# Kernel optimization log

Measured on AMD Instinct MI355X. Metric: run time of the kernel, lower is better.

Reference implementation:

```python
import jax, jax.numpy as jnp
import numpy as np

HID = 128          # args.hid
HEADS = 1          # args.head (forced: concat=True and classifier expects 3*hid)
C = HID            # out_channels per head
ND, NPR, NCL = 4096, 20000, 1024
E_DD, E_DP, E_CP = 500_000, 1_000_000, 500_000
B = 8192
SLOPE = 0.2        # GATConv negative_slope default


def _gat(x_src, x_dst, src, dst, W, a_src, a_dst, bias, num_dst,
         edge_attr=None, W_edge=None, a_edge=None):
    # PyG GATConv: shared lin for src/dst (in_channels is int)
    hs = (x_src @ W).reshape(-1, HEADS, C)            # [Ns,H,C]
    hd = (x_dst @ W).reshape(-1, HEADS, C)            # [Nd,H,C]
    e = jnp.sum(hs * a_src, -1)[src] + jnp.sum(hd * a_dst, -1)[dst]  # [E,H]
    if edge_attr is not None:
        ee = (edge_attr @ W_edge).reshape(-1, HEADS, C)
        e = e + jnp.sum(ee * a_edge, -1)
    e = jnp.where(e > 0, e, SLOPE * e)                # leaky_relu
    emax = jax.ops.segment_max(e, dst, num_segments=num_dst)
    ex = jnp.exp(e - emax[dst])
    denom = jax.ops.segment_sum(ex, dst, num_segments=num_dst)
    alpha = ex / (denom[dst] + 1e-16)                 # PyG softmax eps
    out = jax.ops.segment_sum(hs[src] * alpha[:, :, None], dst, num_segments=num_dst)
    return out.reshape(num_dst, HEADS * C) + bias


def _l2n(x):
    return x / jnp.maximum(jnp.linalg.norm(x, axis=1, keepdims=True), 1e-12)


def setup_inputs() -> dict:
    key = jax.random.key(0)
    ks = iter(jax.random.split(key, 48))

    def nrm(shape, s=0.1):
        return jax.random.normal(next(ks), shape, jnp.float32) * s

    inp = {
        'x_drug': jnp.arange(ND, dtype=jnp.int32),
        'x_protein': jnp.arange(NPR, dtype=jnp.int32),
        'x_cell': jnp.arange(NCL, dtype=jnp.int32),
        'ei_dd': jax.random.randint(next(ks), (2, E_DD), 0, ND),
        'edge_attr_dd': jax.random.normal(next(ks), (E_DD, 1), jnp.float32),
        'src_dp': jax.random.randint(next(ks), (E_DP,), 0, NPR),
        'dst_dp': jax.random.randint(next(ks), (E_DP,), 0, ND),
        'src_cp': jax.random.randint(next(ks), (E_CP,), 0, NPR),
        'dst_cp': jax.random.randint(next(ks), (E_CP,), 0, NCL),
        'drug1': jax.random.randint(next(ks), (B,), 0, ND),
        'drug2': jax.random.randint(next(ks), (B,), 0, ND),
        'cell': jax.random.randint(next(ks), (B,), 0, NCL),
        # embedding tables
        'drug_emb': nrm((ND, HID), 1.0),
        'protein_emb': nrm((NPR, HID), 1.0),
        'cell_emb': nrm((NCL, HID), 1.0),
        # GAT d-d (edge_dim=1)
        'W_dd': nrm((HID, HEADS * C)), 'a_src_dd': nrm((HEADS, C)), 'a_dst_dd': nrm((HEADS, C)),
        'bias_dd': jnp.zeros((HEADS * C,), jnp.float32),
        'W_edge_dd': nrm((1, HEADS * C)), 'a_edge_dd': nrm((HEADS, C)),
        # GAT protein->drug
        'W_dp': nrm((HID, HEADS * C)), 'a_src_dp': nrm((HEADS, C)), 'a_dst_dp': nrm((HEADS, C)),
        'bias_dp': jnp.zeros((HEADS * C,), jnp.float32),
        # GAT protein->cell
        'W_cp': nrm((HID, HEADS * C)), 'a_src_cp': nrm((HEADS, C)), 'a_dst_cp': nrm((HEADS, C)),
        'bias_cp': jnp.zeros((HEADS * C,), jnp.float32),
        # classifier: 3h -> 6h -> 2h -> 2
        'W1': nrm((3 * HID, 6 * HID)), 'b1': jnp.zeros((6 * HID,), jnp.float32),
        'W2': nrm((6 * HID, 2 * HID)), 'b2': jnp.zeros((2 * HID,), jnp.float32),
        'W3': nrm((2 * HID, 2)), 'b3': jnp.zeros((2,), jnp.float32),
    }
    return inp


def reference(x_drug, x_protein, x_cell, ei_dd, edge_attr_dd, src_dp, dst_dp,
              src_cp, dst_cp, drug1, drug2, cell, drug_emb, protein_emb, cell_emb,
              W_dd, a_src_dd, a_dst_dd, bias_dd, W_edge_dd, a_edge_dd,
              W_dp, a_src_dp, a_dst_dp, bias_dp,
              W_cp, a_src_cp, a_dst_cp, bias_cp,
              W1, b1, W2, b2, W3, b3):
    h_d = drug_emb[x_drug]
    h_p = protein_emb[x_protein]
    h_c = cell_emb[x_cell]

    # d-d: add self-loops with edge_attr fill_value='mean' (PyG default)
    src, dst = ei_dd[0], ei_dd[1]
    deg = jax.ops.segment_sum(jnp.ones((E_DD,), jnp.float32), dst, num_segments=ND)
    mean_attr = jax.ops.segment_sum(edge_attr_dd, dst, num_segments=ND) / jnp.maximum(deg, 1.0)[:, None]
    loops = jnp.arange(ND, dtype=src.dtype)
    src2 = jnp.concatenate([src, loops])
    dst2 = jnp.concatenate([dst, loops])
    attr2 = jnp.concatenate([edge_attr_dd, mean_attr], 0)

    out_dd = _gat(h_d, h_d, src2, dst2, W_dd, a_src_dd, a_dst_dd, bias_dd, ND,
                  attr2, W_edge_dd, a_edge_dd)
    out_dp = _gat(h_p, h_d, src_dp, dst_dp, W_dp, a_src_dp, a_dst_dp, bias_dp, ND)
    out_cp = _gat(h_p, h_c, src_cp, dst_cp, W_cp, a_src_cp, a_dst_cp, bias_cp, NCL)

    drug = jax.nn.relu(out_dd + out_dp)   # HeteroConv aggr='sum', then F.relu
    cellx = jax.nn.relu(out_cp)

    hid = jnp.concatenate([_l2n(drug[drug1]), _l2n(drug[drug2]), _l2n(cellx[cell])], 1)
    h = jax.nn.relu(hid @ W1 + b1)        # dropout = identity in eval
    h = jax.nn.relu(h @ W2 + b2)
    return h @ W3 + b3
```

## Files before the change

kernel.cpp:

```cpp
#include <hip/hip_runtime.h>
#include <hip/hip_bf16.h>

#define HIDC 128
typedef __hip_bfloat16 bf16;
typedef __attribute__((ext_vector_type(8))) short short8;
typedef __attribute__((ext_vector_type(4))) float floatx4;

#define CHUNK 4096

__device__ __forceinline__ short f2b(float f) {
    unsigned int u = __builtin_bit_cast(unsigned int, f);
    u += 0x7fff + ((u >> 16) & 1);
    return (short)(u >> 16);
}

__device__ __forceinline__ uint packe(int s, float ev) {
    float w = __expf(ev);
    return ((uint)s << 16) | (uint)(unsigned short)f2b(w);
}

__global__ void __launch_bounds__(256) r15_prep(
    int* __restrict__ zptr, int zwords, int nzb,
    const float* __restrict__ W_dd, const float* __restrict__ W_dp, const float* __restrict__ W_cp,
    const float* __restrict__ a0, const float* __restrict__ a1, const float* __restrict__ a2,
    const float* __restrict__ a3, const float* __restrict__ a4, const float* __restrict__ a5,
    const float* __restrict__ W_edge, const float* __restrict__ a_edge,
    float* __restrict__ wa, float* __restrict__ c_edge,
    const float* __restrict__ W1, short* __restrict__ Wt1, int nT1,
    const float* __restrict__ W2, short* __restrict__ Wt2)
{
    int b = blockIdx.x;
    int tid = threadIdx.x;
    if (b < nzb) {
        int i = b * 256 + tid;
        if (i < zwords) zptr[i] = 0;
        return;
    }
    b -= nzb;
    if (b < 7) {
        __shared__ float as[HIDC];
        int k = tid;
        if (b < 6) {
            const float* W = (b < 2) ? W_dd : (b < 4) ? W_dp : W_cp;
            const float* a = (b == 0) ? a0 : (b == 1) ? a1 : (b == 2) ? a2 : (b == 3) ? a3 : (b == 4) ? a4 : a5;
            if (k < HIDC) as[k] = a[k];
            __syncthreads();
            if (k < HIDC) {
                float s = 0.f;
#pragma unroll 8
                for (int c = 0; c < HIDC; c++) s = fmaf(W[k * HIDC + c], as[c], s);
                wa[b * HIDC + k] = s;
            }
        } else {
            if (k < HIDC) as[k] = W_edge[k] * a_edge[k];
            __syncthreads();
#pragma unroll
            for (int off = 64; off > 0; off >>= 1) { if (k < off) as[k] += as[k + off]; __syncthreads(); }
            if (k == 0) c_edge[0] = as[0];
        }
        return;
    }
    b -= 7;
    const float* W; short* Wt; int K, N, k0, n0;
    if (b < nT1) { W = W1; Wt = Wt1; K = 384; N = 768; k0 = (b / 24) * 32; n0 = (b % 24) * 32; }
    else { b -= nT1; W = W2; Wt = Wt2; K = 768; N = 256; k0 = (b / 8) * 32; n0 = (b % 8) * 32; }
    __shared__ short T[32 * 34];
    int cc = tid & 31, rr = tid >> 5;
#pragma unroll
    for (int it = 0; it < 4; it++) {
        int r = it * 8 + rr;
        T[r * 34 + cc] = f2b(W[(size_t)(k0 + r) * N + n0 + cc]);
    }
    __syncthreads();
#pragma unroll
    for (int it = 0; it < 4; it++) {
        int r = it * 8 + rr;
        Wt[(size_t)(n0 + r) * K + k0 + cc] = T[cc * 34 + r];
    }
}

__global__ void __launch_bounds__(256) r15_scalars(
    const float* __restrict__ drug_emb, const float* __restrict__ prot_emb, const float* __restrict__ cell_emb,
    const int* __restrict__ x_drug, const int* __restrict__ x_prot, const int* __restrict__ x_cell,
    const float* __restrict__ wa,
    float* __restrict__ ssrc_dd, float* __restrict__ sdst_dd, float* __restrict__ sdst_dp,
    float* __restrict__ ssrc_dp, float* __restrict__ ssrc_cp, float* __restrict__ sdst_cp,
    int nd, int npr, int ncl)
{
    int g = blockIdx.x * 4 + (threadIdx.x >> 6);
    int l = threadIdx.x & 63;
    const float2* wa2 = (const float2*)wa;
    if (g < nd) {
        int id = x_drug[g];
        float2 e = ((const float2*)drug_emb)[(size_t)id * 64 + l];
        float2 w0 = wa2[0 * 64 + l], w1 = wa2[1 * 64 + l], w3 = wa2[3 * 64 + l];
        float p0 = e.x * w0.x + e.y * w0.y;
        float p1 = e.x * w1.x + e.y * w1.y;
        float p2 = e.x * w3.x + e.y * w3.y;
#pragma unroll
        for (int off = 32; off > 0; off >>= 1) {
            p0 += __shfl_xor(p0, off, 64);
            p1 += __shfl_xor(p1, off, 64);
            p2 += __shfl_xor(p2, off, 64);
        }
        if (l == 0) { ssrc_dd[g] = p0; sdst_dd[g] = p1; sdst_dp[g] = p2; }
    } else if (g < nd + npr) {
        int r = g - nd;
        int id = x_prot[r];
        float2 e = ((const float2*)prot_emb)[(size_t)id * 64 + l];
        float2 w2 = wa2[2 * 64 + l], w4 = wa2[4 * 64 + l];
        float p0 = e.x * w2.x + e.y * w2.y;
        float p1 = e.x * w4.x + e.y * w4.y;
#pragma unroll
        for (int off = 32; off > 0; off >>= 1) {
            p0 += __shfl_xor(p0, off, 64);
            p1 += __shfl_xor(p1, off, 64);
        }
        if (l == 0) { ssrc_dp[r] = p0; ssrc_cp[r] = p1; }
    } else if (g < nd + npr + ncl) {
        int r = g - nd - npr;
        int id = x_cell[r];
        float2 e = ((const float2*)cell_emb)[(size_t)id * 64 + l];
        float2 w5 = wa2[5 * 64 + l];
        float p0 = e.x * w5.x + e.y * w5.y;
#pragma unroll
        for (int off = 32; off > 0; off >>= 1) p0 += __shfl_xor(p0, off, 64);
        if (l == 0) sdst_cp[r] = p0;
    }
}

__global__ void __launch_bounds__(128) r15_node_gemm(
    const float* __restrict__ drug_emb, const int* __restrict__ x_drug,
    const float* __restrict__ W_dd, bf16* __restrict__ H_dd, int ndb,
    const float* __restrict__ prot_emb, const int* __restrict__ x_prot,
    const float* __restrict__ W_dp, const float* __restrict__ W_cp,
    bf16* __restrict__ H_dp, bf16* __restrict__ H_cp)
{
    __shared__ int ids[16];
    __shared__ float xs[16 * HIDC];
    int bb = blockIdx.x;
    bool isdrug = bb < ndb;
    int r0 = (isdrug ? bb : bb - ndb) * 16;
    const float* emb = isdrug ? drug_emb : prot_emb;
    const int* idx = isdrug ? x_drug : x_prot;
    int tid = threadIdx.x;
    if (tid < 16) ids[tid] = idx[r0 + tid];
    __syncthreads();
    for (int t = tid; t < 16 * HIDC; t += 128) {
        int r = t >> 7, k = t & 127;
        xs[t] = emb[(size_t)ids[r] * HIDC + k];
    }
    __syncthreads();
    int c = tid;
    if (isdrug) {
        float acc[16];
#pragma unroll
        for (int r = 0; r < 16; r++) acc[r] = 0.f;
        for (int k = 0; k < HIDC; k += 4) {
            float w0 = W_dd[(k + 0) * HIDC + c];
            float w1 = W_dd[(k + 1) * HIDC + c];
            float w2 = W_dd[(k + 2) * HIDC + c];
            float w3 = W_dd[(k + 3) * HIDC + c];
#pragma unroll
            for (int r = 0; r < 16; r++) {
                float4 x = *(const float4*)&xs[r * HIDC + k];
                acc[r] = fmaf(x.x, w0, fmaf(x.y, w1, fmaf(x.z, w2, fmaf(x.w, w3, acc[r]))));
            }
        }
#pragma unroll
        for (int r = 0; r < 16; r++) H_dd[(size_t)(r0 + r) * HIDC + c] = __float2bfloat16(acc[r]);
    } else {
        float accA[16], accB[16];
#pragma unroll
        for (int r = 0; r < 16; r++) { accA[r] = 0.f; accB[r] = 0.f; }
        for (int k = 0; k < HIDC; k += 2) {
            float a0 = W_dp[(k + 0) * HIDC + c];
            float a1 = W_dp[(k + 1) * HIDC + c];
            float b0 = W_cp[(k + 0) * HIDC + c];
            float b1 = W_cp[(k + 1) * HIDC + c];
#pragma unroll
            for (int r = 0; r < 16; r++) {
                float2 x = *(const float2*)&xs[r * HIDC + k];
                accA[r] = fmaf(x.x, a0, fmaf(x.y, a1, accA[r]));
                accB[r] = fmaf(x.x, b0, fmaf(x.y, b1, accB[r]));
            }
        }
#pragma unroll
        for (int r = 0; r < 16; r++) {
            H_dp[(size_t)(r0 + r) * HIDC + c] = __float2bfloat16(accA[r]);
            H_cp[(size_t)(r0 + r) * HIDC + c] = __float2bfloat16(accB[r]);
        }
    }
}

__global__ void __launch_bounds__(256) r15_edge_pass1(
    const int* __restrict__ dst_dd, const float* __restrict__ attr_dd, int E_dd, int nb_dd,
    const int* __restrict__ dst_dp, int E_dp, int nb_dp,
    const int* __restrict__ dst_cp, int E_cp,
    int nd, int ncl,
    int* __restrict__ cnt_dd, float* __restrict__ attr_sum,
    int* __restrict__ cnt_dp, int* __restrict__ cnt_cp,
    int* __restrict__ rank_dd, int* __restrict__ rank_dp, int* __restrict__ rank_cp)
{
    __shared__ int lcnt[4096];
    __shared__ float lattr[4096];
    int bid = blockIdx.x;
    const int* dst; const float* attr = nullptr; int E, e0, bins;
    int* gcnt; int* rank;
    if (bid < nb_dd) {
        dst = dst_dd; attr = attr_dd; E = E_dd; e0 = bid * CHUNK; bins = nd;
        gcnt = cnt_dd; rank = rank_dd;
    } else if (bid < nb_dd + nb_dp) {
        dst = dst_dp; E = E_dp; e0 = (bid - nb_dd) * CHUNK; bins = nd;
        gcnt = cnt_dp; rank = rank_dp;
    } else {
        dst = dst_cp; E = E_cp; e0 = (bid - nb_dd - nb_dp) * CHUNK; bins = ncl;
        gcnt = cnt_cp; rank = rank_cp;
    }
    int tid = threadIdx.x;
    for (int b = tid; b < bins; b += 256) { lcnt[b] = 0; if (attr) lattr[b] = 0.f; }
    __syncthreads();
    int e1 = min(e0 + CHUNK, E);
    for (int i = e0 + tid; i < e1; i += 256) {
        int d = dst[i];
        rank[i] = atomicAdd(&lcnt[d], 1);
        if (attr) atomicAdd(&lattr[d], attr[i]);
    }
    __syncthreads();
    for (int b = tid; b < bins; b += 256) {
        int c = lcnt[b];
        if (c > 0) {
            lcnt[b] = atomicAdd(&gcnt[b], c);
            if (attr) atomicAdd(&attr_sum[b], lattr[b]);
        }
    }
    __syncthreads();
    for (int i = e0 + tid; i < e1; i += 256) {
        rank[i] += lcnt[dst[i]];
    }
}

__global__ void __launch_bounds__(1024) r15_exscan3(
    const int* __restrict__ in0, int* __restrict__ out0, int n0,
    const int* __restrict__ in1, int* __restrict__ out1, int n1,
    const int* __restrict__ in2, int* __restrict__ out2, int n2)
{
    const int* in; int* out; int n; int inc;
    if (blockIdx.x == 0)      { in = in0; out = out0; n = n0; inc = 1; }
    else if (blockIdx.x == 1) { in = in1; out = out1; n = n1; inc = 0; }
    else                      { in = in2; out = out2; n = n2; inc = 0; }
    __shared__ int buf[1024];
    __shared__ int carry;
    int tid = threadIdx.x;
    if (tid == 0) carry = 0;
    __syncthreads();
    for (int base = 0; base < n; base += 1024) {
        int i = base + tid;
        int v = (i < n) ? (in[i] + inc) : 0;
        buf[tid] = v; __syncthreads();
        for (int off = 1; off < 1024; off <<= 1) {
            int t = (tid >= off) ? buf[tid - off] : 0;
            __syncthreads();
            buf[tid] += t;
            __syncthreads();
        }
        int c0 = carry;
        int incl = buf[tid];
        if (i < n) out[i] = c0 + incl - v;
        __syncthreads();
        if (tid == 1023) carry = c0 + buf[1023];
        __syncthreads();
    }
    if (tid == 0) out[n] = carry;
}

__global__ void r15_scatter(
    const int* __restrict__ ei_dd, const float* __restrict__ attr_dd, int E_dd, int nd,
    const int* __restrict__ src_dp, const int* __restrict__ dst_dp, int E_dp,
    const int* __restrict__ src_cp, const int* __restrict__ dst_cp, int E_cp,
    const int* __restrict__ rank_dd, const int* __restrict__ rank_dp, const int* __restrict__ rank_cp,
    const int* __restrict__ deg_dd, const float* __restrict__ attr_sum,
    const float* __restrict__ c_edge_ptr,
    const float* __restrict__ ssrc_dd, const float* __restrict__ sdst_dd,
    const float* __restrict__ ssrc_dp, const float* __restrict__ sdst_dp,
    const float* __restrict__ ssrc_cp, const float* __restrict__ sdst_cp,
    const int* __restrict__ rs_dd, const int* __restrict__ rs_dp, const int* __restrict__ rs_cp,
    uint* __restrict__ csr_dd, uint* __restrict__ csr_dp, uint* __restrict__ csr_cp)
{
    int i = blockIdx.x * 256 + threadIdx.x;
    if (i < E_dd) {
        int s = ei_dd[i], d = ei_dd[E_dd + i];
        float ev = ssrc_dd[s] + sdst_dd[d] + attr_dd[i] * c_edge_ptr[0];
        ev = (ev > 0.f) ? ev : 0.2f * ev;
        csr_dd[rs_dd[d] + rank_dd[i]] = packe(s, ev);
        return;
    }
    i -= E_dd;
    if (i < nd) {
        int d = i;
        int dg = deg_dd[d];
        float mean = attr_sum[d] / fmaxf((float)dg, 1.0f);
        float ev = ssrc_dd[d] + sdst_dd[d] + mean * c_edge_ptr[0];
        ev = (ev > 0.f) ? ev : 0.2f * ev;
        csr_dd[rs_dd[d] + dg] = packe(d, ev);
        return;
    }
    i -= nd;
    if (i < E_dp) {
        int d = dst_dp[i], s = src_dp[i];
        float ev = ssrc_dp[s] + sdst_dp[d];
        ev = (ev > 0.f) ? ev : 0.2f * ev;
        csr_dp[rs_dp[d] + rank_dp[i]] = packe(s, ev);
        return;
    }
    i -= E_dp;
    if (i < E_cp) {
        int d = dst_cp[i], s = src_cp[i];
        float ev = ssrc_cp[s] + sdst_cp[d];
        ev = (ev > 0.f) ? ev : 0.2f * ev;
        csr_cp[rs_cp[d] + rank_cp[i]] = packe(s, ev);
    }
}

__global__ void __launch_bounds__(256) r15_agg3(
    const int* __restrict__ rs_dd, const uint* __restrict__ csr_dd, const uint* __restrict__ Hdd,
    float* __restrict__ agg_dd, int nd,
    const int* __restrict__ rs_dp, const uint* __restrict__ csr_dp, const uint* __restrict__ Hdp,
    float* __restrict__ agg_dp,
    const int* __restrict__ rs_cp, const uint* __restrict__ csr_cp, const uint* __restrict__ Hcp,
    float* __restrict__ agg_cp, int R)
{
    int b = blockIdx.x;
    int slot = b & 7;
    int half = slot >> 2;
    int row_g = (b >> 3) * 4 + (slot & 3);
    if (row_g >= R) return;
    const int* rs; const uint* csr; const uint* H2; float* out; int row;
    if (row_g < nd)          { rs = rs_dd; csr = csr_dd; H2 = Hdd; out = agg_dd; row = row_g; }
    else if (row_g < 2 * nd) { rs = rs_dp; csr = csr_dp; H2 = Hdp; out = agg_dp; row = row_g - nd; }
    else                     { rs = rs_cp; csr = csr_cp; H2 = Hcp; out = agg_cp; row = row_g - 2 * nd; }
    int t = threadIdx.x;
    int c2 = t & 15, g = t >> 4;
    int s = rs[row], e = rs[row + 1];

    __shared__ float se[2][128];
    __shared__ int ss[2][128];
    const uint2* Hh = (const uint2*)H2 + half * 16 + c2;
    float acc[4] = {0.f, 0.f, 0.f, 0.f};
    float dsum = 0.f;
    int nchunks = (e - s + 127) >> 7;

    if (nchunks > 0 && t < min(128, e - s)) {
        uint pk = csr[s + t];
        float wv = __uint_as_float((pk & 0xffffu) << 16);
        se[0][t] = wv; ss[0][t] = (int)(pk >> 16);
        dsum += wv;
    }
    __syncthreads();
    for (int kk = 0; kk < nchunks; kk++) {
        int pb = kk & 1;
        if (kk + 1 < nchunks) {
            int nb2 = s + (kk + 1) * 128;
            int nlim = min(128, e - nb2);
            if (t < nlim) {
                uint pk = csr[nb2 + t];
                float wv = __uint_as_float((pk & 0xffffu) << 16);
                se[pb ^ 1][t] = wv; ss[pb ^ 1][t] = (int)(pk >> 16);
                dsum += wv;
            }
        }
        int lim = min(128, e - s - kk * 128);
        if (lim == 128) {
#pragma unroll 8
            for (int jj = 0; jj < 8; jj++) {
                int j = jj * 16 + g;
                uint2 u = Hh[(size_t)ss[pb][j] * 32];
                float w = se[pb][j];
                acc[0] = fmaf(w, __uint_as_float(u.x << 16), acc[0]);
                acc[1] = fmaf(w, __uint_as_float(u.x & 0xffff0000u), acc[1]);
                acc[2] = fmaf(w, __uint_as_float(u.y << 16), acc[2]);
                acc[3] = fmaf(w, __uint_as_float(u.y & 0xffff0000u), acc[3]);
            }
        } else {
            for (int j = g; j < lim; j += 16) {
                uint2 u = Hh[(size_t)ss[pb][j] * 32];
                float w = se[pb][j];
                acc[0] = fmaf(w, __uint_as_float(u.x << 16), acc[0]);
                acc[1] = fmaf(w, __uint_as_float(u.x & 0xffff0000u), acc[1]);
                acc[2] = fmaf(w, __uint_as_float(u.y << 16), acc[2]);
                acc[3] = fmaf(w, __uint_as_float(u.y & 0xffff0000u), acc[3]);
            }
        }
        __syncthreads();
    }

    float dwave = dsum;
#pragma unroll
    for (int off = 32; off > 0; off >>= 1) dwave += __shfl_xor(dwave, off, 64);
#pragma unroll
    for (int i = 0; i < 4; i++) {
        acc[i] += __shfl_xor(acc[i], 16, 64);
        acc[i] += __shfl_xor(acc[i], 32, 64);
    }
    __shared__ float rsum[4][64];
    __shared__ float dred[4];
    int w = t >> 6, l = t & 63;
    if (l == 0) dred[w] = dwave;
    if (l < 16) {
#pragma unroll
        for (int i = 0; i < 4; i++) rsum[w][l * 4 + i] = acc[i];
    }
    __syncthreads();
    if (t < 64) {
        float inv = 1.f / (dred[0] + dred[1] + dred[2] + dred[3] + 1e-16f);
        float v = rsum[0][t] + rsum[1][t] + rsum[2][t] + rsum[3][t];
        out[(size_t)row * HIDC + half * 64 + t] = v * inv;
    }
}

__global__ void __launch_bounds__(128) r15_fuse(
    const float* __restrict__ agg_dd, const float* __restrict__ bias_dd,
    const float* __restrict__ agg_dp, const float* __restrict__ bias_dp,
    float* __restrict__ drugN, int nd,
    const float* __restrict__ agg_cp, const float* __restrict__ bias_cp,
    float* __restrict__ cellN)
{
    int b = blockIdx.x, c = threadIdx.x;
    float v;
    float* outN;
    int d;
    if (b < nd) {
        d = b;
        v = agg_dd[(size_t)d * HIDC + c] + bias_dd[c] + agg_dp[(size_t)d * HIDC + c] + bias_dp[c];
        outN = drugN;
    } else {
        d = b - nd;
        v = agg_cp[(size_t)d * HIDC + c] + bias_cp[c];
        outN = cellN;
    }
    v = fmaxf(v, 0.f);
    __shared__ float red[HIDC];
    red[c] = v * v; __syncthreads();
#pragma unroll
    for (int off = 64; off > 0; off >>= 1) { if (c < off) red[c] += red[c + off]; __syncthreads(); }
    float nrm = fmaxf(sqrtf(red[0]), 1e-12f);
    outN[(size_t)d * HIDC + c] = v / nrm;
}

__global__ void __launch_bounds__(128) r15_gather_hid(
    const float* __restrict__ drugN, const float* __restrict__ cellN,
    const int* __restrict__ d1, const int* __restrict__ d2, const int* __restrict__ ce,
    short* __restrict__ hid)
{
    int b = blockIdx.x, c = threadIdx.x;
    hid[(size_t)b * 384 + c]       = f2b(drugN[(size_t)d1[b] * HIDC + c]);
    hid[(size_t)b * 384 + 128 + c] = f2b(drugN[(size_t)d2[b] * HIDC + c]);
    hid[(size_t)b * 384 + 256 + c] = f2b(cellN[(size_t)ce[b] * HIDC + c]);
}

template <int NB, int OUT_BF16>
__global__ void __launch_bounds__(256) r15_mgemm(
    const short* __restrict__ X, const short* __restrict__ Wt, const float* __restrict__ bias,
    void* __restrict__ Y, int M, int K, int N)
{
    constexpr int BN = NB * 16;
    __shared__ short As[128 * 40];
    __shared__ short Bs[BN * 40];
    int m0 = blockIdx.x * 128, n0 = blockIdx.y * BN;
    int tid = threadIdx.x;
    int w = tid >> 6, lane = tid & 63;
    int q = lane >> 4, t = lane & 15;
    int sr = tid >> 1, sc = tid & 1;

    floatx4 acc[2][NB];
#pragma unroll
    for (int i = 0; i < 2; i++)
#pragma unroll
        for (int c = 0; c < NB; c++) acc[i][c] = (floatx4){0.f, 0.f, 0.f, 0.f};

    for (int kt = 0; kt < K; kt += 32) {
        {
            const uint4* ga = (const uint4*)(X + (size_t)(m0 + sr) * K + kt + sc * 16);
            uint4 a0 = ga[0], a1 = ga[1];
            *(uint4*)&As[sr * 40 + sc * 16]     = a0;
            *(uint4*)&As[sr * 40 + sc * 16 + 8] = a1;
        }
        for (int tt = tid; tt < BN * 2; tt += 256) {
            int r = tt >> 1, h = tt & 1;
            const uint4* gb = (const uint4*)(Wt + (size_t)(n0 + r) * K + kt + h * 16);
            uint4 b0 = gb[0], b1 = gb[1];
            *(uint4*)&Bs[r * 40 + h * 16]     = b0;
            *(uint4*)&Bs[r * 40 + h * 16 + 8] = b1;
        }
        __syncthreads();
        short8 af[2], bf[NB];
#pragma unroll
        for (int i = 0; i < 2; i++)
            af[i] = *(const short8*)&As[(w * 32 + i * 16 + t) * 40 + q * 8];
#pragma unroll
        for (int c = 0; c < NB; c++)
            bf[c] = *(const short8*)&Bs[(c * 16 + t) * 40 + q * 8];
#pragma unroll
        for (int i = 0; i < 2; i++)
#pragma unroll
            for (int c = 0; c < NB; c++)
                acc[i][c] = __builtin_amdgcn_mfma_f32_16x16x32_bf16(af[i], bf[c], acc[i][c], 0, 0, 0);
        __syncthreads();
    }

    float bv[NB];
#pragma unroll
    for (int c = 0; c < NB; c++) bv[c] = bias[n0 + c * 16 + t];
#pragma unroll
    for (int i = 0; i < 2; i++) {
#pragma unroll
        for (int c = 0; c < NB; c++) {
#pragma unroll
            for (int ii = 0; ii < 4; ii++) {
                int m_g = m0 + w * 32 + i * 16 + q * 4 + ii;
                int n_g = n0 + c * 16 + t;
                float v = acc[i][c][ii] + bv[c];
                v = fmaxf(v, 0.f);
                if (OUT_BF16) ((short*)Y)[(size_t)m_g * N + n_g] = f2b(v);
                else          ((float*)Y)[(size_t)m_g * N + n_g] = v;
            }
        }
    }
}

__global__ void __launch_bounds__(256) r15_final(
    const float* __restrict__ h2, const float* __restrict__ W3, const float* __restrict__ b3,
    float* __restrict__ out)
{
    int row = blockIdx.x * 4 + (threadIdx.x >> 6);
    int lane = threadIdx.x & 63;
    float a0 = 0.f, a1 = 0.f;
    for (int k = lane; k < 256; k += 64) {
        float h = h2[(size_t)row * 256 + k];
        a0 = fmaf(h, W3[k * 2 + 0], a0);
        a1 = fmaf(h, W3[k * 2 + 1], a1);
    }
#pragma unroll
    for (int off = 32; off > 0; off >>= 1) {
        a0 += __shfl_down(a0, off, 64);
        a1 += __shfl_down(a1, off, 64);
    }
    if (lane == 0) {
        out[row * 2 + 0] = a0 + b3[0];
        out[row * 2 + 1] = a1 + b3[1];
    }
}

extern "C" void kernel_launch(void* const* d_in, const int* in_sizes, int n_in,
                              void* d_out, int out_size, void* d_ws, size_t ws_size,
                              hipStream_t stream)
{
    const int* x_drug      = (const int*)d_in[0];
    const int* x_protein   = (const int*)d_in[1];
    const int* x_cell      = (const int*)d_in[2];
    const int* ei_dd       = (const int*)d_in[3];
    const float* attr_dd   = (const float*)d_in[4];
    const int* src_dp      = (const int*)d_in[5];
    const int* dst_dp      = (const int*)d_in[6];
    const int* src_cp      = (const int*)d_in[7];
    const int* dst_cp      = (const int*)d_in[8];
    const int* drug1       = (const int*)d_in[9];
    const int* drug2       = (const int*)d_in[10];
    const int* cellb       = (const int*)d_in[11];
    const float* drug_emb  = (const float*)d_in[12];
    const float* protein_emb = (const float*)d_in[13];
    const float* cell_emb  = (const float*)d_in[14];
    const float* W_dd      = (const float*)d_in[15];
    const float* a_src_dd  = (const float*)d_in[16];
    const float* a_dst_dd  = (const float*)d_in[17];
    const float* bias_dd   = (const float*)d_in[18];
    const float* W_edge_dd = (const float*)d_in[19];
    const float* a_edge_dd = (const float*)d_in[20];
    const float* W_dp      = (const float*)d_in[21];
    const float* a_src_dp  = (const float*)d_in[22];
    const float* a_dst_dp  = (const float*)d_in[23];
    const float* bias_dp   = (const float*)d_in[24];
    const float* W_cp      = (const float*)d_in[25];
    const float* a_src_cp  = (const float*)d_in[26];
    const float* a_dst_cp  = (const float*)d_in[27];
    const float* bias_cp   = (const float*)d_in[28];
    const float* W1        = (const float*)d_in[29];
    const float* b1        = (const float*)d_in[30];
    const float* W2        = (const float*)d_in[31];
    const float* b2        = (const float*)d_in[32];
    const float* W3        = (const float*)d_in[33];
    const float* b3        = (const float*)d_in[34];

    const int ND  = in_sizes[0];
    const int NPR = in_sizes[1];
    const int NCL = in_sizes[2];
    const int E_DD = in_sizes[4];
    const int E_DP = in_sizes[5];
    const int E_CP = in_sizes[7];
    const int B    = in_sizes[9];
    const int E_DD2 = E_DD + ND;

    char* p = (char*)d_ws;
    auto carve = [&](size_t bytes) -> char* {
        char* r = p;
        p += (bytes + 255) & ~(size_t)255;
        return r;
    };
    char* zstart = p;
    int*   cnt_dd   = (int*)  carve((size_t)ND * 4);
    float* attr_sum = (float*)carve((size_t)ND * 4);
    int*   cnt_dp   = (int*)  carve((size_t)ND * 4);
    int*   cnt_cp   = (int*)  carve((size_t)NCL * 4);
    size_t zbytes = (size_t)(p - zstart);
    int*   rs_dd    = (int*)  carve((size_t)(ND + 1) * 4);
    int*   rs_dp    = (int*)  carve((size_t)(ND + 1) * 4);
    int*   rs_cp    = (int*)  carve((size_t)(NCL + 1) * 4);
    float* c_edge   = (float*)carve(256);
    float* wa       = (float*)carve(6 * HIDC * 4);
    bf16*  H_dd     = (bf16*) carve((size_t)ND * HIDC * 2);
    bf16*  H_dp     = (bf16*) carve((size_t)NPR * HIDC * 2);
    bf16*  H_cp     = (bf16*) carve((size_t)NPR * HIDC * 2);
    float* ssrc_dd  = (float*)carve((size_t)ND * 4);
    float* sdst_dd  = (float*)carve((size_t)ND * 4);
    float* ssrc_dp  = (float*)carve((size_t)NPR * 4);
    float* sdst_dp  = (float*)carve((size_t)ND * 4);
    float* ssrc_cp  = (float*)carve((size_t)NPR * 4);
    float* sdst_cp  = (float*)carve((size_t)NCL * 4);
    int*   rank_dd  = (int*)  carve((size_t)E_DD * 4);
    int*   rank_dp  = (int*)  carve((size_t)E_DP * 4);
    int*   rank_cp  = (int*)  carve((size_t)E_CP * 4);
    uint*  csr_dd   = (uint*) carve((size_t)E_DD2 * 4);
    uint*  csr_dp   = (uint*) carve((size_t)E_DP * 4);
    uint*  csr_cp   = (uint*) carve((size_t)E_CP * 4);
    float* agg_dd   = (float*)carve((size_t)ND * HIDC * 4);
    float* agg_dp   = (float*)carve((size_t)ND * HIDC * 4);
    float* agg_cp   = (float*)carve((size_t)NCL * HIDC * 4);
    float* drugN    = (float*)carve((size_t)ND * HIDC * 4);
    float* cellN    = (float*)carve((size_t)NCL * HIDC * 4);
    short* hidb     = (short*)carve((size_t)B * 384 * 2);
    short* h1b      = (short*)carve((size_t)B * 768 * 2);
    float* h2       = (float*)carve((size_t)B * 256 * 4);
    short* Wt1      = (short*)carve((size_t)384 * 768 * 2);
    short* Wt2      = (short*)carve((size_t)768 * 256 * 2);

    auto cdiv = [](int a, int b) { return (a + b - 1) / b; };

    int zwords = (int)(zbytes / 4);
    int nzb = cdiv(zwords, 256);
    int nT1 = (384 / 32) * (768 / 32);
    int nT2 = (768 / 32) * (256 / 32);
    r15_prep<<<nzb + 7 + nT1 + nT2, 256, 0, stream>>>(
        (int*)zstart, zwords, nzb,
        W_dd, W_dp, W_cp, a_src_dd, a_dst_dd, a_src_dp, a_dst_dp, a_src_cp, a_dst_cp,
        W_edge_dd, a_edge_dd, wa, c_edge, W1, Wt1, nT1, W2, Wt2);

    r15_node_gemm<<<ND / 16 + NPR / 16, 128, 0, stream>>>(
        drug_emb, x_drug, W_dd, H_dd, ND / 16,
        protein_emb, x_protein, W_dp, W_cp, H_dp, H_cp);
    r15_scalars<<<(ND + NPR + NCL) / 4, 256, 0, stream>>>(
        drug_emb, protein_emb, cell_emb, x_drug, x_protein, x_cell, wa,
        ssrc_dd, sdst_dd, sdst_dp, ssrc_dp, ssrc_cp, sdst_cp, ND, NPR, NCL);

    int nb_dd = cdiv(E_DD, CHUNK), nb_dp = cdiv(E_DP, CHUNK), nb_cp = cdiv(E_CP, CHUNK);
    r15_edge_pass1<<<nb_dd + nb_dp + nb_cp, 256, 0, stream>>>(
        ei_dd + E_DD, attr_dd, E_DD, nb_dd,
        dst_dp, E_DP, nb_dp,
        dst_cp, E_CP,
        ND, NCL,
        cnt_dd, attr_sum, cnt_dp, cnt_cp, rank_dd, rank_dp, rank_cp);
    r15_exscan3<<<3, 1024, 0, stream>>>(cnt_dd, rs_dd, ND, cnt_dp, rs_dp, ND, cnt_cp, rs_cp, NCL);
    r15_scatter<<<cdiv(E_DD + ND + E_DP + E_CP, 256), 256, 0, stream>>>(
        ei_dd, attr_dd, E_DD, ND, src_dp, dst_dp, E_DP, src_cp, dst_cp, E_CP,
        rank_dd, rank_dp, rank_cp, cnt_dd, attr_sum, c_edge,
        ssrc_dd, sdst_dd, ssrc_dp, sdst_dp, ssrc_cp, sdst_cp,
        rs_dd, rs_dp, rs_cp, csr_dd, csr_dp, csr_cp);

    {
        int R = 2 * ND + NCL;
        int G = cdiv(R, 4) * 8;
        r15_agg3<<<G, 256, 0, stream>>>(
            rs_dd, csr_dd, (const uint*)H_dd, agg_dd, ND,
            rs_dp, csr_dp, (const uint*)H_dp, agg_dp,
            rs_cp, csr_cp, (const uint*)H_cp, agg_cp, R);
    }

    r15_fuse<<<ND + NCL, 128, 0, stream>>>(agg_dd, bias_dd, agg_dp, bias_dp, drugN, ND,
                                           agg_cp, bias_cp, cellN);

    r15_gather_hid<<<B, 128, 0, stream>>>(drugN, cellN, drug1, drug2, cellb, hidb);
    {
        dim3 g1(B / 128, 768 / 128);
        r15_mgemm<8, 1><<<g1, 256, 0, stream>>>(hidb, Wt1, b1, (void*)h1b, B, 384, 768);
        dim3 g2(B / 128, 256 / 64);
        r15_mgemm<4, 0><<<g2, 256, 0, stream>>>(h1b, Wt2, b2, (void*)h2, B, 768, 256);
    }
    r15_final<<<B / 4, 256, 0, stream>>>(h2, W3, b3, (float*)d_out);
}
```

Before: 344.9 us.

## Merge edge histogram, node GEMM, weight transpose and scalars into one kernel

Combines four independent kernels (edge pass1 histogram/rank, node projection GEMM, MLP weight transpose, attention scalar dot products) into a single block-dispatched mega kernel. The node GEMM now uses 256-thread blocks covering 32 rows as two 16-row halves. This removes three kernel launches and their serialization gaps, letting independent work overlap across CUs. Trade-off: all blocks reserve 32KB shared memory, which may reduce occupancy for the lighter branches.

```diff
diff --git a/kernel.cpp b/kernel.cpp
--- a/kernel.cpp
+++ b/kernel.cpp
@@ -19,15 +19,13 @@
     return ((uint)s << 16) | (uint)(unsigned short)f2b(w);
 }
 
-__global__ void __launch_bounds__(256) r15_prep(
+__global__ void __launch_bounds__(256) r16_pre(
     int* __restrict__ zptr, int zwords, int nzb,
     const float* __restrict__ W_dd, const float* __restrict__ W_dp, const float* __restrict__ W_cp,
     const float* __restrict__ a0, const float* __restrict__ a1, const float* __restrict__ a2,
     const float* __restrict__ a3, const float* __restrict__ a4, const float* __restrict__ a5,
     const float* __restrict__ W_edge, const float* __restrict__ a_edge,
-    float* __restrict__ wa, float* __restrict__ c_edge,
-    const float* __restrict__ W1, short* __restrict__ Wt1, int nT1,
-    const float* __restrict__ W2, short* __restrict__ Wt2)
+    float* __restrict__ wa, float* __restrict__ c_edge)
 {
     int b = blockIdx.x;
     int tid = threadIdx.x;
@@ -37,210 +35,220 @@
         return;
     }
     b -= nzb;
-    if (b < 7) {
-        __shared__ float as[HIDC];
-        int k = tid;
-        if (b < 6) {
-            const float* W = (b < 2) ? W_dd : (b < 4) ? W_dp : W_cp;
-            const float* a = (b == 0) ? a0 : (b == 1) ? a1 : (b == 2) ? a2 : (b == 3) ? a3 : (b == 4) ? a4 : a5;
-            if (k < HIDC) as[k] = a[k];
-            __syncthreads();
-            if (k < HIDC) {
-                float s = 0.f;
+    __shared__ float as[HIDC];
+    int k = tid;
+    if (b < 6) {
+        const float* W = (b < 2) ? W_dd : (b < 4) ? W_dp : W_cp;
+        const float* a = (b == 0) ? a0 : (b == 1) ? a1 : (b == 2) ? a2 : (b == 3) ? a3 : (b == 4) ? a4 : a5;
+        if (k < HIDC) as[k] = a[k];
+        __syncthreads();
+        if (k < HIDC) {
+            float s = 0.f;
 #pragma unroll 8
-                for (int c = 0; c < HIDC; c++) s = fmaf(W[k * HIDC + c], as[c], s);
-                wa[b * HIDC + k] = s;
-            }
-        } else {
-            if (k < HIDC) as[k] = W_edge[k] * a_edge[k];
-            __syncthreads();
-#pragma unroll
-            for (int off = 64; off > 0; off >>= 1) { if (k < off) as[k] += as[k + off]; __syncthreads(); }
-            if (k == 0) c_edge[0] = as[0];
-        }
-        return;
-    }
-    b -= 7;
-    const float* W; short* Wt; int K, N, k0, n0;
-    if (b < nT1) { W = W1; Wt = Wt1; K = 384; N = 768; k0 = (b / 24) * 32; n0 = (b % 24) * 32; }
-    else { b -= nT1; W = W2; Wt = Wt2; K = 768; N = 256; k0 = (b / 8) * 32; n0 = (b % 8) * 32; }
-    __shared__ short T[32 * 34];
-    int cc = tid & 31, rr = tid >> 5;
-#pragma unroll
-    for (int it = 0; it < 4; it++) {
-        int r = it * 8 + rr;
-        T[r * 34 + cc] = f2b(W[(size_t)(k0 + r) * N + n0 + cc]);
-    }
-    __syncthreads();
-#pragma unroll
-    for (int it = 0; it < 4; it++) {
-        int r = it * 8 + rr;
-        Wt[(size_t)(n0 + r) * K + k0 + cc] = T[cc * 34 + r];
-    }
-}
-
-__global__ void __launch_bounds__(256) r15_scalars(
-    const float* __restrict__ drug_emb, const float* __restrict__ prot_emb, const float* __restrict__ cell_emb,
-    const int* __restrict__ x_drug, const int* __restrict__ x_prot, const int* __restrict__ x_cell,
+            for (int c = 0; c < HIDC; c++) s = fmaf(W[k * HIDC + c], as[c], s);
+            wa[b * HIDC + k] = s;
+        }
+    } else {
+        if (k < HIDC) as[k] = W_edge[k] * a_edge[k];
+        __syncthreads();
+#pragma unroll
+        for (int off = 64; off > 0; off >>= 1) { if (k < off) as[k] += as[k + off]; __syncthreads(); }
+        if (k == 0) c_edge[0] = as[0];
+    }
+}
+
+__global__ void __launch_bounds__(256) r16_mega(
+    const int* __restrict__ dst_dd, const float* __restrict__ attr_dd, int E_dd, int nb_dd,
+    const int* __restrict__ dst_dp, int E_dp, int nb_dp,
+    const int* __restrict__ dst_cp, int E_cp, int nb_cp,
+    int nd, int ncl,
+    int* __restrict__ cnt_dd, float* __restrict__ attr_sum,
+    int* __restrict__ cnt_dp, int* __restrict__ cnt_cp,
+    int* __restrict__ rank_dd, int* __restrict__ rank_dp, int* __restrict__ rank_cp,
+    const float* __restrict__ drug_emb, const int* __restrict__ x_drug,
+    const float* __restrict__ W_dd, bf16* __restrict__ H_dd, int ndb32,
+    const float* __restrict__ prot_emb, const int* __restrict__ x_prot,
+    const float* __restrict__ W_dp, const float* __restrict__ W_cp,
+    bf16* __restrict__ H_dp, bf16* __restrict__ H_cp, int npb32,
+    const float* __restrict__ W1, short* __restrict__ Wt1, int nT1,
+    const float* __restrict__ W2, short* __restrict__ Wt2, int nT2,
+    const float* __restrict__ cell_emb, const int* __restrict__ x_cell,
     const float* __restrict__ wa,
     float* __restrict__ ssrc_dd, float* __restrict__ sdst_dd, float* __restrict__ sdst_dp,
     float* __restrict__ ssrc_dp, float* __restrict__ ssrc_cp, float* __restrict__ sdst_cp,
-    int nd, int npr, int ncl)
-{
-    int g = blockIdx.x * 4 + (threadIdx.x >> 6);
-    int l = threadIdx.x & 63;
-    const float2* wa2 = (const float2*)wa;
-    if (g < nd) {
-        int id = x_drug[g];
-        float2 e = ((const float2*)drug_emb)[(size_t)id * 64 + l];
-        float2 w0 = wa2[0 * 64 + l], w1 = wa2[1 * 64 + l], w3 = wa2[3 * 64 + l];
-        float p0 = e.x * w0.x + e.y * w0.y;
-        float p1 = e.x * w1.x + e.y * w1.y;
-        float p2 = e.x * w3.x + e.y * w3.y;
-#pragma unroll
-        for (int off = 32; off > 0; off >>= 1) {
-            p0 += __shfl_xor(p0, off, 64);
-            p1 += __shfl_xor(p1, off, 64);
-            p2 += __shfl_xor(p2, off, 64);
-        }
-        if (l == 0) { ssrc_dd[g] = p0; sdst_dd[g] = p1; sdst_dp[g] = p2; }
-    } else if (g < nd + npr) {
-        int r = g - nd;
-        int id = x_prot[r];
-        float2 e = ((const float2*)prot_emb)[(size_t)id * 64 + l];
-        float2 w2 = wa2[2 * 64 + l], w4 = wa2[4 * 64 + l];
-        float p0 = e.x * w2.x + e.y * w2.y;
-        float p1 = e.x * w4.x + e.y * w4.y;
-#pragma unroll
-        for (int off = 32; off > 0; off >>= 1) {
-            p0 += __shfl_xor(p0, off, 64);
-            p1 += __shfl_xor(p1, off, 64);
-        }
-        if (l == 0) { ssrc_dp[r] = p0; ssrc_cp[r] = p1; }
-    } else if (g < nd + npr + ncl) {
-        int r = g - nd - npr;
-        int id = x_cell[r];
-        float2 e = ((const float2*)cell_emb)[(size_t)id * 64 + l];
-        float2 w5 = wa2[5 * 64 + l];
-        float p0 = e.x * w5.x + e.y * w5.y;
-#pragma unroll
-        for (int off = 32; off > 0; off >>= 1) p0 += __shfl_xor(p0, off, 64);
-        if (l == 0) sdst_cp[r] = p0;
-    }
-}
-
-__global__ void __launch_bounds__(128) r15_node_gemm(
-    const float* __restrict__ drug_emb, const int* __restrict__ x_drug,
-    const float* __restrict__ W_dd, bf16* __restrict__ H_dd, int ndb,
-    const float* __restrict__ prot_emb, const int* __restrict__ x_prot,
-    const float* __restrict__ W_dp, const float* __restrict__ W_cp,
-    bf16* __restrict__ H_dp, bf16* __restrict__ H_cp)
-{
-    __shared__ int ids[16];
-    __shared__ float xs[16 * HIDC];
-    int bb = blockIdx.x;
-    bool isdrug = bb < ndb;
-    int r0 = (isdrug ? bb : bb - ndb) * 16;
-    const float* emb = isdrug ? drug_emb : prot_emb;
-    const int* idx = isdrug ? x_drug : x_prot;
+    int npr)
+{
+    __shared__ int smem[8192];
+    int b = blockIdx.x;
     int tid = threadIdx.x;
-    if (tid < 16) ids[tid] = idx[r0 + tid];
-    __syncthreads();
-    for (int t = tid; t < 16 * HIDC; t += 128) {
-        int r = t >> 7, k = t & 127;
-        xs[t] = emb[(size_t)ids[r] * HIDC + k];
-    }
-    __syncthreads();
-    int c = tid;
-    if (isdrug) {
-        float acc[16];
-#pragma unroll
-        for (int r = 0; r < 16; r++) acc[r] = 0.f;
-        for (int k = 0; k < HIDC; k += 4) {
-            float w0 = W_dd[(k + 0) * HIDC + c];
-            float w1 = W_dd[(k + 1) * HIDC + c];
-            float w2 = W_dd[(k + 2) * HIDC + c];
-            float w3 = W_dd[(k + 3) * HIDC + c];
+    int nb_pass = nb_dd + nb_dp + nb_cp;
+
+    if (b < nb_pass) {
+        int* lcnt = smem;
+        float* lattr = (float*)(smem + 4096);
+        const int* dst; const float* attr = nullptr; int E, e0, bins;
+        int* gcnt; int* rank;
+        if (b < nb_dd) {
+            dst = dst_dd; attr = attr_dd; E = E_dd; e0 = b * CHUNK; bins = nd;
+            gcnt = cnt_dd; rank = rank_dd;
+        } else if (b < nb_dd + nb_dp) {
+            dst = dst_dp; E = E_dp; e0 = (b - nb_dd) * CHUNK; bins = nd;
+            gcnt = cnt_dp; rank = rank_dp;
+        } else {
+            dst = dst_cp; E = E_cp; e0 = (b - nb_dd - nb_dp) * CHUNK; bins = ncl;
+            gcnt = cnt_cp; rank = rank_cp;
+        }
+        for (int bb = tid; bb < bins; bb += 256) { lcnt[bb] = 0; if (attr) lattr[bb] = 0.f; }
+        __syncthreads();
+        int e1 = min(e0 + CHUNK, E);
+        for (int i = e0 + tid; i < e1; i += 256) {
+            int d = dst[i];
+            rank[i] = atomicAdd(&lcnt[d], 1);
+            if (attr) atomicAdd(&lattr[d], attr[i]);
+        }
+        __syncthreads();
+        for (int bb = tid; bb < bins; bb += 256) {
+            int c = lcnt[bb];
+            if (c > 0) {
+                lcnt[bb] = atomicAdd(&gcnt[bb], c);
+                if (attr) atomicAdd(&attr_sum[bb], lattr[bb]);
+            }
+        }
+        __syncthreads();
+        for (int i = e0 + tid; i < e1; i += 256) {
+            rank[i] += lcnt[dst[i]];
+        }
+        return;
+    }
+    b -= nb_pass;
+
+    if (b < ndb32 + npb32) {
+        int* ids = smem;
+        float* xs = (float*)(smem + 32);
+        bool isdrug = b < ndb32;
+        int r0 = (isdrug ? b : b - ndb32) * 32;
+        const float* emb = isdrug ? drug_emb : prot_emb;
+        const int* idx = isdrug ? x_drug : x_prot;
+        if (tid < 32) ids[tid] = idx[r0 + tid];
+        __syncthreads();
+        for (int t = tid; t < 32 * HIDC; t += 256) {
+            int r = t >> 7, k = t & 127;
+            xs[t] = emb[(size_t)ids[r] * HIDC + k];
+        }
+        __syncthreads();
+        int c = tid & 127, h = tid >> 7;
+        const float* xb = xs + (h * 16) * HIDC;
+        int rbase = r0 + h * 16;
+        if (isdrug) {
+            float acc[16];
+#pragma unroll
+            for (int r = 0; r < 16; r++) acc[r] = 0.f;
+            for (int k = 0; k < HIDC; k += 4) {
+                float w0 = W_dd[(k + 0) * HIDC + c];
+                float w1 = W_dd[(k + 1) * HIDC + c];
+                float w2 = W_dd[(k + 2) * HIDC + c];
+                float w3 = W_dd[(k + 3) * HIDC + c];
+#pragma unroll
+                for (int r = 0; r < 16; r++) {
+                    float4 x = *(const float4*)&xb[r * HIDC + k];
+                    acc[r] = fmaf(x.x, w0, fmaf(x.y, w1, fmaf(x.z, w2, fmaf(x.w, w3, acc[r]))));
+                }
+            }
+#pragma unroll
+            for (int r = 0; r < 16; r++)
+                H_dd[(size_t)(rbase + r) * HIDC + c] = __float2bfloat16(acc[r]);
+        } else {
+            float accA[16], accB[16];
+#pragma unroll
+            for (int r = 0; r < 16; r++) { accA[r] = 0.f; accB[r] = 0.f; }
+            for (int k = 0; k < HIDC; k += 2) {
+                float a0 = W_dp[(k + 0) * HIDC + c];
+                float a1 = W_dp[(k + 1) * HIDC + c];
+                float b0 = W_cp[(k + 0) * HIDC + c];
+                float b1 = W_cp[(k + 1) * HIDC + c];
+#pragma unroll
+                for (int r = 0; r < 16; r++) {
+                    float2 x = *(const float2*)&xb[r * HIDC + k];
+                    accA[r] = fmaf(x.x, a0, fmaf(x.y, a1, accA[r]));
+                    accB[r] = fmaf(x.x, b0, fmaf(x.y, b1, accB[r]));
+                }
+            }
 #pragma unroll
             for (int r = 0; r < 16; r++) {
-                float4 x = *(const float4*)&xs[r * HIDC + k];
-                acc[r] = fmaf(x.x, w0, fmaf(x.y, w1, fmaf(x.z, w2, fmaf(x.w, w3, acc[r]))));
-            }
-        }
-#pragma unroll
-        for (int r = 0; r < 16; r++) H_dd[(size_t)(r0 + r) * HIDC + c] = __float2bfloat16(acc[r]);
-    } else {
-        float accA[16], accB[16];
-#pragma unroll
-        for (int r = 0; r < 16; r++) { accA[r] = 0.f; accB[r] = 0.f; }
-        for (int k = 0; k < HIDC; k += 2) {
-            float a0 = W_dp[(k + 0) * HIDC + c];
-            float a1 = W_dp[(k + 1) * HIDC + c];
-            float b0 = W_cp[(k + 0) * HIDC + c];
-            float b1 = W_cp[(k + 1) * HIDC + c];
-#pragma unroll
-            for (int r = 0; r < 16; r++) {
-                float2 x = *(const float2*)&xs[r * HIDC + k];
-                accA[r] = fmaf(x.x, a0, fmaf(x.y, a1, accA[r]));
-                accB[r] = fmaf(x.x, b0, fmaf(x.y, b1, accB[r]));
-            }
-        }
-#pragma unroll
-        for (int r = 0; r < 16; r++) {
-            H_dp[(size_t)(r0 + r) * HIDC + c] = __float2bfloat16(accA[r]);
-            H_cp[(size_t)(r0 + r) * HIDC + c] = __float2bfloat16(accB[r]);
-        }
-    }
-}
-
-__global__ void __launch_bounds__(256) r15_edge_pass1(
-    const int* __restrict__ dst_dd, const float* __restrict__ attr_dd, int E_dd, int nb_dd,
-    const int* __restrict__ dst_dp, int E_dp, int nb_dp,
-    const int* __restrict__ dst_cp, int E_cp,
-    int nd, int ncl,
-    int* __restrict__ cnt_dd, float* __restrict__ attr_sum,
-    int* __restrict__ cnt_dp, int* __restrict__ cnt_cp,
-    int* __restrict__ rank_dd, int* __restrict__ rank_dp, int* __restrict__ rank_cp)
-{
-    __shared__ int lcnt[4096];
-    __shared__ float lattr[4096];
-    int bid = blockIdx.x;
-    const int* dst; const float* attr = nullptr; int E, e0, bins;
-    int* gcnt; int* rank;
-    if (bid < nb_dd) {
-        dst = dst_dd; attr = attr_dd; E = E_dd; e0 = bid * CHUNK; bins = nd;
-        gcnt = cnt_dd; rank = rank_dd;
-    } else if (bid < nb_dd + nb_dp) {
-        dst = dst_dp; E = E_dp; e0 = (bid - nb_dd) * CHUNK; bins = nd;
-        gcnt = cnt_dp; rank = rank_dp;
-    } else {
-        dst = dst_cp; E = E_cp; e0 = (bid - nb_dd - nb_dp) * CHUNK; bins = ncl;
-        gcnt = cnt_cp; rank = rank_cp;
-    }
-    int tid = threadIdx.x;
-    for (int b = tid; b < bins; b += 256) { lcnt[b] = 0; if (attr) lattr[b] = 0.f; }
-    __syncthreads();
-    int e1 = min(e0 + CHUNK, E);
-    for (int i = e0 + tid; i < e1; i += 256) {
-        int d = dst[i];
-        rank[i] = atomicAdd(&lcnt[d], 1);
-        if (attr) atomicAdd(&lattr[d], attr[i]);
-    }
-    __syncthreads();
-    for (int b = tid; b < bins; b += 256) {
-        int c = lcnt[b];
-        if (c > 0) {
-            lcnt[b] = atomicAdd(&gcnt[b], c);
-            if (attr) atomicAdd(&attr_sum[b], lattr[b]);
-        }
-    }
-    __syncthreads();
-    for (int i = e0 + tid; i < e1; i += 256) {
-        rank[i] += lcnt[dst[i]];
-    }
-}
-
-__global__ void __launch_bounds__(1024) r15_exscan3(
+                H_dp[(size_t)(rbase + r) * HIDC + c] = __float2bfloat16(accA[r]);
+                H_cp[(size_t)(rbase + r) * HIDC + c] = __float2bfloat16(accB[r]);
+            }
+        }
+        return;
+    }
+    b -= ndb32 + npb32;
+
+    if (b < nT1 + nT2) {
+        short* T = (short*)smem;
+        const float* W; short* Wt; int K, N, k0, n0;
+        if (b < nT1) { W = W1; Wt = Wt1; K = 384; N = 768; k0 = (b / 24) * 32; n0 = (b % 24) * 32; }
+        else { b -= nT1; W = W2; Wt = Wt2; K = 768; N = 256; k0 = (b / 8) * 32; n0 = (b % 8) * 32; }
+        int cc = tid & 31, rr = tid >> 5;
+#pragma unroll
+        for (int it = 0; it < 4; it++) {
+            int r = it * 8 + rr;
+            T[r * 34 + cc] = f2b(W[(size_t)(k0 + r) * N + n0 + cc]);
+        }
+        __syncthreads();
+#pragma unroll
+        for (int it = 0; it < 4; it++) {
+            int r = it * 8 + rr;
+            Wt[(size_t)(n0 + r) * K + k0 + cc] = T[cc * 34 + r];
+        }
+        return;
+    }
+    b -= nT1 + nT2;
+
+    {
+        int g = b * 4 + (tid >> 6);
+        int l = tid & 63;
+        const float2* wa2 = (const float2*)wa;
+        if (g < nd) {
+            int id = x_drug[g];
+            float2 e = ((const float2*)drug_emb)[(size_t)id * 64 + l];
+            float2 w0 = wa2[0 * 64 + l], w1 = wa2[1 * 64 + l], w3 = wa2[3 * 64 + l];
+            float p0 = e.x * w0.x + e.y * w0.y;
+            float p1 = e.x * w1.x + e.y * w1.y;
+            float p2 = e.x * w3.x + e.y * w3.y;
+#pragma unroll
+            for (int off = 32; off > 0; off >>= 1) {
+                p0 += __shfl_xor(p0, off, 64);
+                p1 += __shfl_xor(p1, off, 64);
+                p2 += __shfl_xor(p2, off, 64);
+            }
+            if (l == 0) { ssrc_dd[g] = p0; sdst_dd[g] = p1; sdst_dp[g] = p2; }
+        } else if (g < nd + npr) {
+            int r = g - nd;
+            int id = x_prot[r];
+            float2 e = ((const float2*)prot_emb)[(size_t)id * 64 + l];
+            float2 w2 = wa2[2 * 64 + l], w4 = wa2[4 * 64 + l];
+            float p0 = e.x * w2.x + e.y * w2.y;
+            float p1 = e.x * w4.x + e.y * w4.y;
+#pragma unroll
+            for (int off = 32; off > 0; off >>= 1) {
+                p0 += __shfl_xor(p0, off, 64);
+                p1 += __shfl_xor(p1, off, 64);
+            }
+            if (l == 0) { ssrc_dp[r] = p0; ssrc_cp[r] = p1; }
+        } else if (g < nd + npr + ncl) {
+            int r = g - nd - npr;
+            int id = x_cell[r];
+            float2 e = ((const float2*)cell_emb)[(size_t)id * 64 + l];
+            float2 w5 = wa2[5 * 64 + l];
+            float p0 = e.x * w5.x + e.y * w5.y;
+#pragma unroll
+            for (int off = 32; off > 0; off >>= 1) p0 += __shfl_xor(p0, off, 64);
+            if (l == 0) sdst_cp[r] = p0;
+        }
+    }
+}
+
+__global__ void __launch_bounds__(1024) r16_exscan3(
     const int* __restrict__ in0, int* __restrict__ out0, int n0,
     const int* __restrict__ in1, int* __restrict__ out1, int n1,
     const int* __restrict__ in2, int* __restrict__ out2, int n2)
@@ -274,7 +282,7 @@
     if (tid == 0) out[n] = carry;
 }
 
-__global__ void r15_scatter(
+__global__ void r16_scatter(
     const int* __restrict__ ei_dd, const float* __restrict__ attr_dd, int E_dd, int nd,
     const int* __restrict__ src_dp, const int* __restrict__ dst_dp, int E_dp,
     const int* __restrict__ src_cp, const int* __restrict__ dst_cp, int E_cp,
@@ -322,7 +330,7 @@
     }
 }
 
-__global__ void __launch_bounds__(256) r15_agg3(
+__global__ void __launch_bounds__(256) r16_agg3(
     const int* __restrict__ rs_dd, const uint* __restrict__ csr_dd, const uint* __restrict__ Hdd,
     float* __restrict__ agg_dd, int nd,
     const int* __restrict__ rs_dp, const uint* __restrict__ csr_dp, const uint* __restrict__ Hdp,
@@ -418,7 +426,7 @@
     }
 }
 
-__global__ void __launch_bounds__(128) r15_fuse(
+__global__ void __launch_bounds__(128) r16_fuse(
     const float* __restrict__ agg_dd, const float* __restrict__ bias_dd,
     const float* __restrict__ agg_dp, const float* __restrict__ bias_dp,
     float* __restrict__ drugN, int nd,
@@ -447,7 +455,7 @@
     outN[(size_t)d * HIDC + c] = v / nrm;
 }
 
-__global__ void __launch_bounds__(128) r15_gather_hid(
+__global__ void __launch_bounds__(128) r16_gather_hid(
     const float* __restrict__ drugN, const float* __restrict__ cellN,
     const int* __restrict__ d1, const int* __restrict__ d2, const int* __restrict__ ce,
     short* __restrict__ hid)
@@ -459,7 +467,7 @@
 }
 
 template <int NB, int OUT_BF16>
-__global__ void __launch_bounds__(256) r15_mgemm(
+__global__ void __launch_bounds__(256) r16_mgemm(
     const short* __restrict__ X, const short* __restrict__ Wt, const float* __restrict__ bias,
     void* __restrict__ Y, int M, int K, int N)
 {
@@ -528,7 +536,7 @@
     }
 }
 
-__global__ void __launch_bounds__(256) r15_final(
+__global__ void __launch_bounds__(256) r16_final(
     const float* __restrict__ h2, const float* __restrict__ W3, const float* __restrict__ b3,
     float* __restrict__ out)
 {
@@ -647,29 +655,30 @@
 
     int zwords = (int)(zbytes / 4);
     int nzb = cdiv(zwords, 256);
+    r16_pre<<<nzb + 7, 256, 0, stream>>>(
+        (int*)zstart, zwords, nzb,
+        W_dd, W_dp, W_cp, a_src_dd, a_dst_dd, a_src_dp, a_dst_dp, a_src_cp, a_dst_cp,
+        W_edge_dd, a_edge_dd, wa, c_edge);
+
+    int nb_dd = cdiv(E_DD, CHUNK), nb_dp = cdiv(E_DP, CHUNK), nb_cp = cdiv(E_CP, CHUNK);
+    int ndb32 = ND / 32, npb32 = NPR / 32;
     int nT1 = (384 / 32) * (768 / 32);
     int nT2 = (768 / 32) * (256 / 32);
-    r15_prep<<<nzb + 7 + nT1 + nT2, 256, 0, stream>>>(
-        (int*)zstart, zwords, nzb,
-        W_dd, W_dp, W_cp, a_src_dd, a_dst_dd, a_src_dp, a_dst_dp, a_src_cp, a_dst_cp,
-        W_edge_dd, a_edge_dd, wa, c_edge, W1, Wt1, nT1, W2, Wt2);
-
-    r15_node_gemm<<<ND / 16 + NPR / 16, 128, 0, stream>>>(
-        drug_emb, x_drug, W_dd, H_dd, ND / 16,
-        protein_emb, x_protein, W_dp, W_cp, H_dp, H_cp);
-    r15_scalars<<<(ND + NPR + NCL) / 4, 256, 0, stream>>>(
-        drug_emb, protein_emb, cell_emb, x_drug, x_protein, x_cell, wa,
-        ssrc_dd, sdst_dd, sdst_dp, ssrc_dp, ssrc_cp, sdst_cp, ND, NPR, NCL);
-
-    int nb_dd = cdiv(E_DD, CHUNK), nb_dp = cdiv(E_DP, CHUNK), nb_cp = cdiv(E_CP, CHUNK);
-    r15_edge_pass1<<<nb_dd + nb_dp + nb_cp, 256, 0, stream>>>(
+    int nsc = (ND + NPR + NCL) / 4;
+    r16_mega<<<nb_dd + nb_dp + nb_cp + ndb32 + npb32 + nT1 + nT2 + nsc, 256, 0, stream>>>(
         ei_dd + E_DD, attr_dd, E_DD, nb_dd,
         dst_dp, E_DP, nb_dp,
-        dst_cp, E_CP,
+        dst_cp, E_CP, nb_cp,
         ND, NCL,
-        cnt_dd, attr_sum, cnt_dp, cnt_cp, rank_dd, rank_dp, rank_cp);
-    r15_exscan3<<<3, 1024, 0, stream>>>(cnt_dd, rs_dd, ND, cnt_dp, rs_dp, ND, cnt_cp, rs_cp, NCL);
-    r15_scatter<<<cdiv(E_DD + ND + E_DP + E_CP, 256), 256, 0, stream>>>(
+        cnt_dd, attr_sum, cnt_dp, cnt_cp, rank_dd, rank_dp, rank_cp,
+        drug_emb, x_drug, W_dd, H_dd, ndb32,
+        protein_emb, x_protein, W_dp, W_cp, H_dp, H_cp, npb32,
+        W1, Wt1, nT1, W2, Wt2, nT2,
+        cell_emb, x_cell, wa,
+        ssrc_dd, sdst_dd, sdst_dp, ssrc_dp, ssrc_cp, sdst_cp, NPR);
+
+    r16_exscan3<<<3, 1024, 0, stream>>>(cnt_dd, rs_dd, ND, cnt_dp, rs_dp, ND, cnt_cp, rs_cp, NCL);
+    r16_scatter<<<cdiv(E_DD + ND + E_DP + E_CP, 256), 256, 0, stream>>>(
         ei_dd, attr_dd, E_DD, ND, src_dp, dst_dp, E_DP, src_cp, dst_cp, E_CP,
         rank_dd, rank_dp, rank_cp, cnt_dd, attr_sum, c_edge,
         ssrc_dd, sdst_dd, ssrc_dp, sdst_dp, ssrc_cp, sdst_cp,
@@ -678,21 +687,21 @@
     {
         int R = 2 * ND + NCL;
         int G = cdiv(R, 4) * 8;
-        r15_agg3<<<G, 256, 0, stream>>>(
+        r16_agg3<<<G, 256, 0, stream>>>(
             rs_dd, csr_dd, (const uint*)H_dd, agg_dd, ND,
             rs_dp, csr_dp, (const uint*)H_dp, agg_dp,
             rs_cp, csr_cp, (const uint*)H_cp, agg_cp, R);
     }
 
-    r15_fuse<<<ND + NCL, 128, 0, stream>>>(agg_dd, bias_dd, agg_dp, bias_dp, drugN, ND,
+    r16_fuse<<<ND + NCL, 128, 0, stream>>>(agg_dd, bias_dd, agg_dp, bias_dp, drugN, ND,
                                            agg_cp, bias_cp, cellN);
 
-    r15_gather_hid<<<B, 128, 0, stream>>>(drugN, cellN, drug1, drug2, cellb, hidb);
+    r16_gather_hid<<<B, 128, 0, stream>>>(drugN, cellN, drug1, drug2, cellb, hidb);
     {
         dim3 g1(B / 128, 768 / 128);
-        r15_mgemm<8, 1><<<g1, 256, 0, stream>>>(hidb, Wt1, b1, (void*)h1b, B, 384, 768);
+        r16_mgemm<8, 1><<<g1, 256, 0, stream>>>(hidb, Wt1, b1, (void*)h1b, B, 384, 768);
         dim3 g2(B / 128, 256 / 64);
-        r15_mgemm<4, 0><<<g2, 256, 0, stream>>>(h1b, Wt2, b2, (void*)h2, B, 768, 256);
-    }
-    r15_final<<<B / 4, 256, 0, stream>>>(h2, W3, b3, (float*)d_out);
-}
+        r16_mgemm<4, 0><<<g2, 256, 0, stream>>>(h1b, Wt2, b2, (void*)h2, B, 768, 256);
+    }
+    r16_final<<<B / 4, 256, 0, stream>>>(h2, W3, b3, (float*)d_out);
+}
```

Result: faster. 316.8 us (-8.2%).
